# Kernel tuning notes

Hardware: AMD Instinct MI355X
Metric: run time of the kernel (lower is better)

The kernel has to match this reference:

```python
import jax, jax.numpy as jnp
import numpy as np

N_TOKENS = 16384
DIM = 4096
NUM_EXPERTS = 128
TOP_K = 8


def setup_inputs() -> dict:
    key = jax.random.key(0)
    k1, k2 = jax.random.split(key)
    x = jax.random.normal(k1, (N_TOKENS, DIM), dtype=jnp.float32)
    gate_w = jax.random.normal(k2, (NUM_EXPERTS, DIM), dtype=jnp.float32) * (DIM ** -0.5)
    return {"x": x, "gate_w": gate_w, "experts_per_token": TOP_K, "num_experts": NUM_EXPERTS}


def reference(x, gate_w, experts_per_token, num_experts):
    # gate: x @ W^T -> (N, E) logits
    scores = jnp.einsum('nd,ed->ne', x, gate_w)
    # softmax in fp32, cast back to input dtype
    probs = jax.nn.softmax(scores.astype(jnp.float32), axis=-1).astype(x.dtype)
    # stable descending argsort (argsort of negated probs, stable)
    sorted_indices = jnp.argsort(-probs, axis=1, stable=True)
    selected_experts = sorted_indices[:, :experts_per_token]            # (N, k)
    top_scores = jnp.take_along_axis(probs, selected_experts, axis=1)   # (N, k)
    # norm_topk_prob=True: renormalize selected weights to sum to 1
    denom = jnp.clip(top_scores.sum(axis=-1, keepdims=True), 1e-8, None)
    top_scores = top_scores / denom
    flat_experts = selected_experts.reshape(-1)                         # (N*k,)
    num_tokens_per_expert = jnp.bincount(flat_experts, length=num_experts)
    # stable sort token-slots by expert id for expert grouping
    perm = jnp.argsort(flat_experts, stable=True)                       # (N*k,)
    top_scores_sorted = top_scores.reshape(-1)[perm]
    token_indices = perm // experts_per_token
    return top_scores_sorted, token_indices, num_tokens_per_expert
```

## Files before the change

### kernel.cpp

```cpp
#include <hip/hip_runtime.h>
#include <math.h>

typedef _Float16 f16;
typedef f16 f16x8 __attribute__((ext_vector_type(8)));
typedef float f32x4 __attribute__((ext_vector_type(4)));

#define NT    16384
#define DIM   4096
#define NEXP  128
#define TOPK  8
#define NFLAT (NT * TOPK)
#define SBLK  512
#define KS    2
#define KPER  (DIM / KS)
#define BK    64
#define NST   (KPER / BK)
#define BT    128

#define COUNTS_OFF 0
#define SEL_OFF    1024
#define WGT_OFF    (SEL_OFF + NFLAT * 4)
#define BH_OFF     (WGT_OFF + NFLAT * 4)
#define BO_OFF     (BH_OFF + NEXP * SBLK * 4)
#define WPK_OFF    (BO_OFF + NEXP * SBLK * 4)
#define PART_OFF   (WPK_OFF + NEXP * DIM * 4)

#define G1P __attribute__((address_space(1)))
#define L3P __attribute__((address_space(3)))

__device__ __forceinline__ void gload_lds16(const void* g, void* l) {
    __builtin_amdgcn_global_load_lds((const G1P unsigned int*)g,
                                     (L3P unsigned int*)l, 16, 0, 0);
}

__device__ __forceinline__ void split2(float v, f16& h, f16& m) {
    h = (f16)v;
    m = (f16)((v - (float)h) * 2048.0f);
}

__global__ __launch_bounds__(256)
void wsplit_kernel(const float* __restrict__ gw, char* __restrict__ wpk) {
    const int t = blockIdx.x * 256 + threadIdx.x;
    const int l = t & 63, kkc = (t >> 6) & 1, g = (t >> 7) & 7, st = t >> 10;
    const int e = g * 16 + (l & 15);
    const int k0 = st * 64 + kkc * 32 + (l >> 4) * 8;
    float4 a = *(const float4*)&gw[e * 4096 + k0];
    float4 b = *(const float4*)&gw[e * 4096 + k0 + 4];
    union { f16 f[8]; uint4 u; } ph, pm;
    split2(a.x * 64.f, ph.f[0], pm.f[0]); split2(a.y * 64.f, ph.f[1], pm.f[1]);
    split2(a.z * 64.f, ph.f[2], pm.f[2]); split2(a.w * 64.f, ph.f[3], pm.f[3]);
    split2(b.x * 64.f, ph.f[4], pm.f[4]); split2(b.y * 64.f, ph.f[5], pm.f[5]);
    split2(b.z * 64.f, ph.f[6], pm.f[6]); split2(b.w * 64.f, ph.f[7], pm.f[7]);
    const size_t base = ((size_t)(st * 8 + g) * 4 + kkc) * 1024 + l * 16;
    *(uint4*)(wpk + base)        = ph.u;
    *(uint4*)(wpk + base + 2048) = pm.u;
}

__global__ __launch_bounds__(512, 2)
void gemm_kernel(const float* __restrict__ x, const char* __restrict__ wpk,
                 float* __restrict__ partial) {
    __shared__ __align__(16) char smem[131072];
    char* WB = smem + 65536;

    const int tid  = threadIdx.x;
    const int bid  = blockIdx.x;
    const int ks   = bid & 1;
    const int tok0 = (bid >> 1) * BT;
    const int lane = tid & 63, wid = tid >> 6;
    const int r = wid >> 2, eg = wid & 3;
    const int fr = lane & 15, hi = lane >> 4;

    const int s8  = tid >> 3;
    const int skq = (tid & 7) * 8;
    const int xkk = skq >> 5, xhi = (skq >> 3) & 3;
    int xwb[2];
#pragma unroll
    for (int p = 0; p < 2; ++p) {
        const int srow = p * 64 + s8;
        const int xi = srow >> 4, xfr = srow & 15;
        const int slot = xhi * 16 + xfr;
        xwb[p] = ((xi * 2 + xkk) * 64 + (slot ^ ((slot >> 4) << 1))) * 16;
    }
    const int lxs = (lane ^ ((lane >> 4) << 1)) * 16;

    f32x4 acc0[4][2], acc1[4][2];
#pragma unroll
    for (int i = 0; i < 4; ++i)
#pragma unroll
        for (int j = 0; j < 2; ++j) {
            acc0[i][j] = (f32x4){0.f, 0.f, 0.f, 0.f};
            acc1[i][j] = (f32x4){0.f, 0.f, 0.f, 0.f};
        }

    const float* xbase = x + (size_t)(tok0 + s8) * DIM + ks * KPER + skq;
    const char*  bsrc0 = wpk + ((size_t)(ks * NST) * 8 + wid) * 4096 + lane * 16;

#define XLOAD(XR, ST) { \
    _Pragma("unroll") \
    for (int p = 0; p < 2; ++p) { \
        const float* pp = xbase + (size_t)p * 64 * DIM + (size_t)(ST) * BK; \
        XR[p][0] = *(const float4*)pp; \
        XR[p][1] = *(const float4*)(pp + 4); \
    } }
#define W_PREF(ST, B) { \
    const char* wsrc = bsrc0 + (size_t)(ST) * 8 * 4096; \
    char* wdst = WB + (B) * 32768 + wid * 4096; \
    gload_lds16(wsrc,        wdst); \
    gload_lds16(wsrc + 1024, wdst + 1024); \
    gload_lds16(wsrc + 2048, wdst + 2048); \
    gload_lds16(wsrc + 3072, wdst + 3072); }
#define STAGE(CUR, XR) { \
    _Pragma("unroll") \
    for (int p = 0; p < 2; ++p) { \
        union { f16 f[8]; f16x8 v; } ph, pm; \
        split2(XR[p][0].x, ph.f[0], pm.f[0]); split2(XR[p][0].y, ph.f[1], pm.f[1]); \
        split2(XR[p][0].z, ph.f[2], pm.f[2]); split2(XR[p][0].w, ph.f[3], pm.f[3]); \
        split2(XR[p][1].x, ph.f[4], pm.f[4]); split2(XR[p][1].y, ph.f[5], pm.f[5]); \
        split2(XR[p][1].z, ph.f[6], pm.f[6]); split2(XR[p][1].w, ph.f[7], pm.f[7]); \
        *(f16x8*)(smem + (CUR) * 16384 + xwb[p]) = ph.v; \
        *(f16x8*)(smem + 32768 + (CUR) * 16384 + xwb[p]) = pm.v; \
    } }
#define COMPUTE(CUR) { \
    _Pragma("unroll") \
    for (int kk = 0; kk < 2; ++kk) { \
        f16x8 ah[4], am[4]; \
        _Pragma("unroll") \
        for (int i = 0; i < 4; ++i) { \
            const int xb = (CUR) * 16384 + (((r * 4 + i) * 2 + kk) * 64) * 16 + lxs; \
            ah[i] = *(const f16x8*)(smem + xb); \
            am[i] = *(const f16x8*)(smem + 32768 + xb); \
        } \
        _Pragma("unroll") \
        for (int j = 0; j < 2; ++j) { \
            const int wb = (CUR) * 32768 + (2 * eg + j) * 4096 + kk * 1024 + lane * 16; \
            f16x8 bhf = *(const f16x8*)(WB + wb); \
            f16x8 bmf = *(const f16x8*)(WB + wb + 2048); \
            _Pragma("unroll") \
            for (int i = 0; i < 4; ++i) { \
                acc0[i][j] = __builtin_amdgcn_mfma_f32_16x16x32_f16(ah[i], bhf, acc0[i][j], 0, 0, 0); \
                acc1[i][j] = __builtin_amdgcn_mfma_f32_16x16x32_f16(ah[i], bmf, acc1[i][j], 0, 0, 0); \
                acc1[i][j] = __builtin_amdgcn_mfma_f32_16x16x32_f16(am[i], bhf, acc1[i][j], 0, 0, 0); \
            } \
        } \
    } }
#define STEP(CUR, XRC, XRP, PX, PW, SI, VMSTR) { \
    STAGE(CUR, XRC); \
    asm volatile("s_waitcnt lgkmcnt(0) vmcnt(" VMSTR ")" ::: "memory"); \
    __builtin_amdgcn_s_barrier(); \
    __builtin_amdgcn_sched_barrier(0); \
    if (PW) { W_PREF((SI) + 1, (CUR) ^ 1); } \
    if (PX) { XLOAD(XRC, (SI) + 2); } \
    __builtin_amdgcn_s_setprio(1); \
    COMPUTE(CUR); \
    __builtin_amdgcn_s_setprio(0); }

    float4 xr0[2][2], xr1[2][2];
    W_PREF(0, 0);
    XLOAD(xr0, 0);
    XLOAD(xr1, 1);

    for (int st = 0; st < 30; st += 2) {
        STEP(0, xr0, xr1, 1, 1, st, "4");
        STEP(1, xr1, xr0, 1, 1, st + 1, "4");
    }
    STEP(0, xr0, xr1, 0, 1, 30, "4");
    STEP(1, xr1, xr0, 0, 0, 31, "0");

    float* pbase = partial + ((size_t)ks * NT + tok0 + r * 64) * NEXP;
#pragma unroll
    for (int i = 0; i < 4; ++i)
#pragma unroll
        for (int j = 0; j < 2; ++j)
#pragma unroll
            for (int q = 0; q < 4; ++q) {
                const int row = i * 16 + hi * 4 + q;
                const int e   = eg * 32 + j * 16 + fr;
                pbase[(size_t)row * NEXP + e] =
                    (acc0[i][j][q] + acc1[i][j][q] * (1.0f / 2048.0f)) * (1.0f / 64.0f);
            }
}

__global__ __launch_bounds__(256)
void topk_kernel(const float* __restrict__ partial, float* __restrict__ wgt,
                 int* __restrict__ sel, int* __restrict__ counts,
                 int* __restrict__ bh) {
    __shared__ float S[32][132];
    __shared__ int h[NEXP];
    const int tid = threadIdx.x;
    const int tok0 = blockIdx.x * 32;
    const int tok = tid >> 3, c = tid & 7;

    f32x4 s0 = {0, 0, 0, 0}, s1 = {0, 0, 0, 0}, s2 = {0, 0, 0, 0}, s3 = {0, 0, 0, 0};
#pragma unroll
    for (int ksq = 0; ksq < KS; ++ksq) {
        const float* p = partial + ((size_t)ksq * NT + tok0 + tok) * NEXP + c * 16;
        s0 += *(const f32x4*)(p);
        s1 += *(const f32x4*)(p + 4);
        s2 += *(const f32x4*)(p + 8);
        s3 += *(const f32x4*)(p + 12);
    }
    *(f32x4*)&S[tok][c * 16]      = s0;
    *(f32x4*)&S[tok][c * 16 + 4]  = s1;
    *(f32x4*)&S[tok][c * 16 + 8]  = s2;
    *(f32x4*)&S[tok][c * 16 + 12] = s3;
    if (tid < NEXP) h[tid] = 0;
    __syncthreads();

    if (tid < 32) {
        float bs[8]; int bi[8];
#pragma unroll
        for (int q = 0; q < 8; ++q) { bs[q] = -3.0e38f; bi[q] = 0; }
        for (int e = 0; e < NEXP; ++e) {
            float s = S[tid][e];
            if (s > bs[7]) {
                int pos = 7;
#pragma unroll
                for (int q = 6; q >= 0; q--) pos = (s > bs[q]) ? q : pos;
#pragma unroll
                for (int q = 7; q >= 1; q--) {
                    bool sh = (q > pos);
                    bs[q] = sh ? bs[q - 1] : bs[q];
                    bi[q] = sh ? bi[q - 1] : bi[q];
                }
#pragma unroll
                for (int q = 0; q < 8; q++)
                    if (q == pos) { bs[q] = s; bi[q] = e; }
            }
        }
        float m = bs[0], sum = 0.f, ex[8];
#pragma unroll
        for (int q = 0; q < 8; ++q) { ex[q] = expf(bs[q] - m); sum += ex[q]; }
        float inv = 1.f / fmaxf(sum, 1e-8f);
        const int tok_g = tok0 + tid;
#pragma unroll
        for (int q = 0; q < 8; ++q) {
            wgt[tok_g * TOPK + q] = ex[q] * inv;
            sel[tok_g * TOPK + q] = bi[q];
            atomicAdd(&h[bi[q]], 1);
        }
    }
    __syncthreads();
    if (tid < NEXP) {
        int cc = h[tid];
        bh[tid * SBLK + blockIdx.x] = cc;
        if (cc) atomicAdd(&counts[tid], cc);
    }
}

__global__ void scan_kernel(const int* __restrict__ bh, const int* __restrict__ counts,
                            int* __restrict__ bo, float* __restrict__ out) {
    const int e = blockIdx.x, tid = threadIdx.x;
    __shared__ int pre[NEXP];
    __shared__ int wsum[8];
    if (tid < NEXP) pre[tid] = counts[tid];
    __syncthreads();
#pragma unroll
    for (int d = 1; d < NEXP; d <<= 1) {
        int o = (tid < NEXP && tid >= d) ? pre[tid - d] : 0;
        __syncthreads();
        if (tid < NEXP) pre[tid] += o;
        __syncthreads();
    }
    const int gb = (e == 0) ? 0 : pre[e - 1];
    if (tid == 0) out[2 * NFLAT + e] = (float)counts[e];

    const int lane = tid & 63, wid = tid >> 6;
    int v = bh[e * SBLK + tid];
    int sc = v;
#pragma unroll
    for (int d = 1; d < 64; d <<= 1) {
        int o = __shfl_up(sc, d);
        sc += (lane >= d) ? o : 0;
    }
    if (lane == 63) wsum[wid] = sc;
    __syncthreads();
    int add = 0;
#pragma unroll
    for (int ww = 0; ww < 8; ww++) add += (ww < wid) ? wsum[ww] : 0;
    bo[e * SBLK + tid] = gb + sc - v + add;
}

__global__ void scatter_kernel(const int* __restrict__ sel, const float* __restrict__ wgt,
                               const int* __restrict__ bo, float* __restrict__ out) {
    const int tid = threadIdx.x, b = blockIdx.x;
    const int i = b * 256 + tid;
    const int e = sel[i];
    const int lane = tid & 63, wid = tid >> 6;
    unsigned long long m = ~0ull;
#pragma unroll
    for (int bit = 0; bit < 7; bit++) {
        unsigned long long bal = __ballot((e >> bit) & 1);
        m &= ((e >> bit) & 1) ? bal : ~bal;
    }
    unsigned long long lower = (lane == 0) ? 0ull : (~0ull >> (64 - lane));
    int wrank = __popcll(m & lower);

    __shared__ int wh_[4][NEXP];
    ((int*)wh_)[tid] = 0; ((int*)wh_)[tid + 256] = 0;
    __syncthreads();
    if (wrank == 0) wh_[wid][e] = __popcll(m);
    __syncthreads();
    int off = 0;
#pragma unroll
    for (int ww = 0; ww < 4; ww++) off += (ww < wid) ? wh_[ww][e] : 0;

    int pos = bo[e * SBLK + b] + off + wrank;
    out[pos] = wgt[i];
    out[NFLAT + pos] = (float)(i >> 3);
}

extern "C" void kernel_launch(void* const* d_in, const int* in_sizes, int n_in,
                              void* d_out, int out_size, void* d_ws, size_t ws_size,
                              hipStream_t stream) {
    const float* x  = (const float*)d_in[0];
    const float* gw = (const float*)d_in[1];
    float* out = (float*)d_out;
    char*  ws  = (char*)d_ws;

    int*   counts  = (int*)(ws + COUNTS_OFF);
    int*   sel     = (int*)(ws + SEL_OFF);
    float* wgt     = (float*)(ws + WGT_OFF);
    int*   bh      = (int*)(ws + BH_OFF);
    int*   bo      = (int*)(ws + BO_OFF);
    char*  wpk     = ws + WPK_OFF;
    float* partial = (float*)(ws + PART_OFF);

    hipMemsetAsync(counts, 0, NEXP * sizeof(int), stream);

    wsplit_kernel<<<256, 256, 0, stream>>>(gw, wpk);
    gemm_kernel<<<256, 512, 0, stream>>>(x, wpk, partial);
    topk_kernel<<<512, 256, 0, stream>>>(partial, wgt, sel, counts, bh);
    scan_kernel<<<NEXP, 512, 0, stream>>>(bh, counts, bo, out);
    scatter_kernel<<<SBLK, 256, 0, stream>>>(sel, wgt, bo, out);
}
```

Baseline: 126.9 us.

## Shrink GEMM tile to 32 tokens and 32-wide K steps for more blocks

Cuts the gate GEMM block tile from 128 to 32 tokens and the K stage from 64 to 32, using 256-thread blocks with 4 blocks per CU and 1024 blocks instead of 256. The weight pre-pack layout is changed to match the new 32-wide K stages, and LDS use per block drops sharply. The aim is more resident waves per CU for better latency hiding and a fuller grid. The cost is that every block now streams the full packed weight for only 32 tokens, so weight traffic from L2 rises fourfold, and the number of pipeline barriers doubles.

```diff
diff --git a/kernel.cpp b/kernel.cpp
--- a/kernel.cpp
+++ b/kernel.cpp
@@ -13,9 +13,9 @@
 #define SBLK  512
 #define KS    2
 #define KPER  (DIM / KS)
-#define BK    64
+#define BK    32
 #define NST   (KPER / BK)
-#define BT    128
+#define BT    32
 
 #define COUNTS_OFF 0
 #define SEL_OFF    1024
@@ -41,9 +41,9 @@
 __global__ __launch_bounds__(256)
 void wsplit_kernel(const float* __restrict__ gw, char* __restrict__ wpk) {
     const int t = blockIdx.x * 256 + threadIdx.x;
-    const int l = t & 63, kkc = (t >> 6) & 1, g = (t >> 7) & 7, st = t >> 10;
+    const int l = t & 63, g = (t >> 6) & 7, st = t >> 9;
     const int e = g * 16 + (l & 15);
-    const int k0 = st * 64 + kkc * 32 + (l >> 4) * 8;
+    const int k0 = st * 32 + (l >> 4) * 8;
     float4 a = *(const float4*)&gw[e * 4096 + k0];
     float4 b = *(const float4*)&gw[e * 4096 + k0 + 4];
     union { f16 f[8]; uint4 u; } ph, pm;
@@ -51,124 +51,104 @@
     split2(a.z * 64.f, ph.f[2], pm.f[2]); split2(a.w * 64.f, ph.f[3], pm.f[3]);
     split2(b.x * 64.f, ph.f[4], pm.f[4]); split2(b.y * 64.f, ph.f[5], pm.f[5]);
     split2(b.z * 64.f, ph.f[6], pm.f[6]); split2(b.w * 64.f, ph.f[7], pm.f[7]);
-    const size_t base = ((size_t)(st * 8 + g) * 4 + kkc) * 1024 + l * 16;
+    const size_t base = (size_t)(st * 8 + g) * 2048 + l * 16;
     *(uint4*)(wpk + base)        = ph.u;
-    *(uint4*)(wpk + base + 2048) = pm.u;
-}
-
-__global__ __launch_bounds__(512, 2)
+    *(uint4*)(wpk + base + 1024) = pm.u;
+}
+
+__global__ __launch_bounds__(256, 4)
 void gemm_kernel(const float* __restrict__ x, const char* __restrict__ wpk,
                  float* __restrict__ partial) {
-    __shared__ __align__(16) char smem[131072];
-    char* WB = smem + 65536;
+    __shared__ __align__(16) char smem[40960];
+    char* WB = smem + 8192;
 
     const int tid  = threadIdx.x;
     const int bid  = blockIdx.x;
     const int ks   = bid & 1;
     const int tok0 = (bid >> 1) * BT;
-    const int lane = tid & 63, wid = tid >> 6;
-    const int r = wid >> 2, eg = wid & 3;
+    const int lane = tid & 63, eg = tid >> 6;
     const int fr = lane & 15, hi = lane >> 4;
 
-    const int s8  = tid >> 3;
-    const int skq = (tid & 7) * 8;
-    const int xkk = skq >> 5, xhi = (skq >> 3) & 3;
-    int xwb[2];
-#pragma unroll
-    for (int p = 0; p < 2; ++p) {
-        const int srow = p * 64 + s8;
-        const int xi = srow >> 4, xfr = srow & 15;
-        const int slot = xhi * 16 + xfr;
-        xwb[p] = ((xi * 2 + xkk) * 64 + (slot ^ ((slot >> 4) << 1))) * 16;
-    }
+    const int srow = tid >> 3;
+    const int xi = srow >> 4, xfr = srow & 15;
+    const int xhi = (tid & 7) >> 1;
+    const int xslot = xhi * 16 + xfr;
+    const int xwb = xi * 1024 + (xslot ^ ((xslot >> 4) << 1)) * 16 + (tid & 1) * 8;
     const int lxs = (lane ^ ((lane >> 4) << 1)) * 16;
 
-    f32x4 acc0[4][2], acc1[4][2];
-#pragma unroll
-    for (int i = 0; i < 4; ++i)
+    f32x4 acc0[2][2], acc1[2][2];
+#pragma unroll
+    for (int i = 0; i < 2; ++i)
 #pragma unroll
         for (int j = 0; j < 2; ++j) {
             acc0[i][j] = (f32x4){0.f, 0.f, 0.f, 0.f};
             acc1[i][j] = (f32x4){0.f, 0.f, 0.f, 0.f};
         }
 
-    const float* xbase = x + (size_t)(tok0 + s8) * DIM + ks * KPER + skq;
-    const char*  bsrc0 = wpk + ((size_t)(ks * NST) * 8 + wid) * 4096 + lane * 16;
-
-#define XLOAD(XR, ST) { \
+    const float* xbase = x + (size_t)(tok0 + srow) * DIM + ks * KPER + (tid & 7) * 4;
+    const char*  bsrc0 = wpk + (size_t)(ks * NST * 8) * 2048 + lane * 16;
+
+#define XLOAD(XR, ST) { XR = *(const float4*)(xbase + (size_t)(ST) * BK); }
+#define W_PREF(ST, B) { \
     _Pragma("unroll") \
-    for (int p = 0; p < 2; ++p) { \
-        const float* pp = xbase + (size_t)p * 64 * DIM + (size_t)(ST) * BK; \
-        XR[p][0] = *(const float4*)pp; \
-        XR[p][1] = *(const float4*)(pp + 4); \
+    for (int c = 0; c < 2; ++c) { \
+        const char* wsrc = bsrc0 + (size_t)((ST) * 8 + 2 * eg + c) * 2048; \
+        char* wdst = WB + (B) * 16384 + (2 * eg + c) * 2048; \
+        gload_lds16(wsrc,        wdst); \
+        gload_lds16(wsrc + 1024, wdst + 1024); \
     } }
-#define W_PREF(ST, B) { \
-    const char* wsrc = bsrc0 + (size_t)(ST) * 8 * 4096; \
-    char* wdst = WB + (B) * 32768 + wid * 4096; \
-    gload_lds16(wsrc,        wdst); \
-    gload_lds16(wsrc + 1024, wdst + 1024); \
-    gload_lds16(wsrc + 2048, wdst + 2048); \
-    gload_lds16(wsrc + 3072, wdst + 3072); }
 #define STAGE(CUR, XR) { \
+    union { f16 f[4]; uint2 u; } ph, pm; \
+    split2(XR.x, ph.f[0], pm.f[0]); split2(XR.y, ph.f[1], pm.f[1]); \
+    split2(XR.z, ph.f[2], pm.f[2]); split2(XR.w, ph.f[3], pm.f[3]); \
+    *(uint2*)(smem + (CUR) * 2048 + xwb) = ph.u; \
+    *(uint2*)(smem + 4096 + (CUR) * 2048 + xwb) = pm.u; }
+#define COMPUTE(CUR) { \
+    f16x8 ah[2], am[2]; \
     _Pragma("unroll") \
-    for (int p = 0; p < 2; ++p) { \
-        union { f16 f[8]; f16x8 v; } ph, pm; \
-        split2(XR[p][0].x, ph.f[0], pm.f[0]); split2(XR[p][0].y, ph.f[1], pm.f[1]); \
-        split2(XR[p][0].z, ph.f[2], pm.f[2]); split2(XR[p][0].w, ph.f[3], pm.f[3]); \
-        split2(XR[p][1].x, ph.f[4], pm.f[4]); split2(XR[p][1].y, ph.f[5], pm.f[5]); \
-        split2(XR[p][1].z, ph.f[6], pm.f[6]); split2(XR[p][1].w, ph.f[7], pm.f[7]); \
-        *(f16x8*)(smem + (CUR) * 16384 + xwb[p]) = ph.v; \
-        *(f16x8*)(smem + 32768 + (CUR) * 16384 + xwb[p]) = pm.v; \
-    } }
-#define COMPUTE(CUR) { \
+    for (int i = 0; i < 2; ++i) { \
+        const int xb = (CUR) * 2048 + i * 1024 + lxs; \
+        ah[i] = *(const f16x8*)(smem + xb); \
+        am[i] = *(const f16x8*)(smem + 4096 + xb); \
+    } \
     _Pragma("unroll") \
-    for (int kk = 0; kk < 2; ++kk) { \
-        f16x8 ah[4], am[4]; \
+    for (int j = 0; j < 2; ++j) { \
+        const int wb = (CUR) * 16384 + (2 * eg + j) * 2048 + lane * 16; \
+        f16x8 bhf = *(const f16x8*)(WB + wb); \
+        f16x8 bmf = *(const f16x8*)(WB + wb + 1024); \
         _Pragma("unroll") \
-        for (int i = 0; i < 4; ++i) { \
-            const int xb = (CUR) * 16384 + (((r * 4 + i) * 2 + kk) * 64) * 16 + lxs; \
-            ah[i] = *(const f16x8*)(smem + xb); \
-            am[i] = *(const f16x8*)(smem + 32768 + xb); \
-        } \
-        _Pragma("unroll") \
-        for (int j = 0; j < 2; ++j) { \
-            const int wb = (CUR) * 32768 + (2 * eg + j) * 4096 + kk * 1024 + lane * 16; \
-            f16x8 bhf = *(const f16x8*)(WB + wb); \
-            f16x8 bmf = *(const f16x8*)(WB + wb + 2048); \
-            _Pragma("unroll") \
-            for (int i = 0; i < 4; ++i) { \
-                acc0[i][j] = __builtin_amdgcn_mfma_f32_16x16x32_f16(ah[i], bhf, acc0[i][j], 0, 0, 0); \
-                acc1[i][j] = __builtin_amdgcn_mfma_f32_16x16x32_f16(ah[i], bmf, acc1[i][j], 0, 0, 0); \
-                acc1[i][j] = __builtin_amdgcn_mfma_f32_16x16x32_f16(am[i], bhf, acc1[i][j], 0, 0, 0); \
-            } \
+        for (int i = 0; i < 2; ++i) { \
+            acc0[i][j] = __builtin_amdgcn_mfma_f32_16x16x32_f16(ah[i], bhf, acc0[i][j], 0, 0, 0); \
+            acc1[i][j] = __builtin_amdgcn_mfma_f32_16x16x32_f16(ah[i], bmf, acc1[i][j], 0, 0, 0); \
+            acc1[i][j] = __builtin_amdgcn_mfma_f32_16x16x32_f16(am[i], bhf, acc1[i][j], 0, 0, 0); \
         } \
     } }
-#define STEP(CUR, XRC, XRP, PX, PW, SI, VMSTR) { \
-    STAGE(CUR, XRC); \
+#define STEP(CUR, XR, PX, PW, SI, VMSTR) { \
+    STAGE(CUR, XR); \
     asm volatile("s_waitcnt lgkmcnt(0) vmcnt(" VMSTR ")" ::: "memory"); \
     __builtin_amdgcn_s_barrier(); \
     __builtin_amdgcn_sched_barrier(0); \
     if (PW) { W_PREF((SI) + 1, (CUR) ^ 1); } \
-    if (PX) { XLOAD(XRC, (SI) + 2); } \
+    if (PX) { XLOAD(XR, (SI) + 2); } \
     __builtin_amdgcn_s_setprio(1); \
     COMPUTE(CUR); \
     __builtin_amdgcn_s_setprio(0); }
 
-    float4 xr0[2][2], xr1[2][2];
+    float4 xr0, xr1;
     W_PREF(0, 0);
     XLOAD(xr0, 0);
     XLOAD(xr1, 1);
 
-    for (int st = 0; st < 30; st += 2) {
-        STEP(0, xr0, xr1, 1, 1, st, "4");
-        STEP(1, xr1, xr0, 1, 1, st + 1, "4");
-    }
-    STEP(0, xr0, xr1, 0, 1, 30, "4");
-    STEP(1, xr1, xr0, 0, 0, 31, "0");
-
-    float* pbase = partial + ((size_t)ks * NT + tok0 + r * 64) * NEXP;
-#pragma unroll
-    for (int i = 0; i < 4; ++i)
+    for (int st = 0; st < 62; st += 2) {
+        STEP(0, xr0, 1, 1, st, "1");
+        STEP(1, xr1, 1, 1, st + 1, "1");
+    }
+    STEP(0, xr0, 0, 1, 62, "1");
+    STEP(1, xr1, 0, 0, 63, "0");
+
+    float* pbase = partial + ((size_t)ks * NT + tok0) * NEXP;
+#pragma unroll
+    for (int i = 0; i < 2; ++i)
 #pragma unroll
         for (int j = 0; j < 2; ++j)
 #pragma unroll
@@ -328,7 +308,7 @@
     hipMemsetAsync(counts, 0, NEXP * sizeof(int), stream);
 
     wsplit_kernel<<<256, 256, 0, stream>>>(gw, wpk);
-    gemm_kernel<<<256, 512, 0, stream>>>(x, wpk, partial);
+    gemm_kernel<<<1024, 256, 0, stream>>>(x, wpk, partial);
     topk_kernel<<<512, 256, 0, stream>>>(partial, wgt, sel, counts, bh);
     scan_kernel<<<NEXP, 512, 0, stream>>>(bh, counts, bo, out);
     scatter_kernel<<<SBLK, 256, 0, stream>>>(sel, wgt, bo, out);
```

After: 149.0 us. 17.3% more time.
